# Performance work log

Hardware: AMD Instinct MI355X
Metric: run time of the kernel (lower is better)

The kernel has to match this reference:

```python
import jax, jax.numpy as jnp
import numpy as np

B, S, D = 1, 2048, 1024
E, K, FF = 8, 2, 4096


def setup_inputs() -> dict:
    key = jax.random.key(0)
    ks = jax.random.split(key, 5)
    scale = 1.0 / np.sqrt(D)
    return {
        "hidden_states": jax.random.normal(ks[0], (B, S, D), dtype=jnp.float32),
        "gate_w": jax.random.normal(ks[1], (E, D), dtype=jnp.float32) * scale,
        "w1": jax.random.normal(ks[2], (E, FF, D), dtype=jnp.float32) * scale,
        "w3": jax.random.normal(ks[3], (E, FF, D), dtype=jnp.float32) * scale,
        "w2": jax.random.normal(ks[4], (E, D, FF), dtype=jnp.float32) * (1.0 / np.sqrt(FF)),
    }


def reference(hidden_states, gate_w, w1, w3, w2):
    b, s, d = hidden_states.shape
    h = hidden_states.reshape(-1, d)                       # [T, D]
    T = h.shape[0]

    router_logits = h @ gate_w.T                           # [T, E]
    rw = jax.nn.softmax(router_logits.astype(jnp.float32), axis=-1)
    top_w, top_idx = jax.lax.top_k(rw, K)                  # [T, K]
    top_w = top_w / jnp.sum(top_w, axis=-1, keepdims=True)
    top_w = top_w.astype(h.dtype)

    # combine weights per (token, expert): zero for non-selected experts
    cw = jnp.zeros((T, E), dtype=h.dtype)
    cw = cw.at[jnp.arange(T)[:, None], top_idx].set(top_w)  # [T, E]

    # dense per-expert gated MLP (E is a small fixed set)
    up = jnp.einsum('td,efd->tef', h, w1)                  # [T, E, FF]
    gt = jnp.einsum('td,efd->tef', h, w3)
    inter = jax.nn.silu(up) * gt
    out_e = jnp.einsum('tef,edf->ted', inter, w2)          # [T, E, D]
    out = jnp.einsum('ted,te->td', out_e, cw)              # [T, D]

    return out.reshape(b, s, d), router_logits
```

## Files before the change

kernel.cpp:

```cpp
#include <hip/hip_runtime.h>
#include <hip/hip_bf16.h>
#include <math.h>

#define T_      2048
#define D_      1024
#define E_      8
#define FF_     4096

typedef __attribute__((ext_vector_type(8))) short  bf16x8;
typedef __attribute__((ext_vector_type(4))) float  f32x4;
typedef __attribute__((ext_vector_type(4))) __bf16 b16x4;

static __device__ inline void async_copy16(const void* g, void* l) {
    __builtin_amdgcn_global_load_lds(
        (const __attribute__((address_space(1))) unsigned int*)g,
        (__attribute__((address_space(3))) unsigned int*)l, 16, 0, 0);
}

__global__ __launch_bounds__(256) void cvt_kernel(
    const float4* __restrict__ src, b16x4* __restrict__ dst, int n4)
{
    int i = blockIdx.x * 256 + threadIdx.x;
    int stride = gridDim.x * 256;
    for (; i < n4; i += stride) {
        float4 v = src[i];
        f32x4 vv; vv[0] = v.x; vv[1] = v.y; vv[2] = v.z; vv[3] = v.w;
        dst[i] = __builtin_convertvector(vv, b16x4);
    }
}

__global__ __launch_bounds__(256) void router_kernel(
    const float* __restrict__ h, const float* __restrict__ gw,
    __bf16* __restrict__ hbf, float* __restrict__ logits,
    int* __restrict__ counts, int* __restrict__ lists, float* __restrict__ wlist)
{
    int t = blockIdx.x * 4 + (threadIdx.x >> 6);
    int lane = threadIdx.x & 63;
    const float4* hrow = (const float4*)(h + (size_t)t * D_);
    const float4* gw4  = (const float4*)gw;
    float part[E_];
#pragma unroll
    for (int e = 0; e < E_; ++e) part[e] = 0.f;
#pragma unroll 4
    for (int i = lane; i < 256; i += 64) {
        float4 v = hrow[i];
        f32x4 vv; vv[0] = v.x; vv[1] = v.y; vv[2] = v.z; vv[3] = v.w;
        b16x4 bv = __builtin_convertvector(vv, b16x4);
        *(b16x4*)(hbf + (size_t)t * D_ + i * 4) = bv;
#pragma unroll
        for (int e = 0; e < E_; ++e) {
            float4 g = gw4[e * 256 + i];
            part[e] += v.x * g.x + v.y * g.y + v.z * g.z + v.w * g.w;
        }
    }
#pragma unroll
    for (int e = 0; e < E_; ++e) {
        float v = part[e];
#pragma unroll
        for (int off = 32; off > 0; off >>= 1) v += __shfl_down(v, off, 64);
        part[e] = v;
    }
    if (lane == 0) {
        float* lo = logits + (size_t)t * E_;
#pragma unroll
        for (int e = 0; e < E_; ++e) lo[e] = part[e];
        int i0 = 0;
#pragma unroll
        for (int e = 1; e < E_; ++e) if (part[e] > part[i0]) i0 = e;
        int i1 = (i0 == 0) ? 1 : 0;
#pragma unroll
        for (int e = 0; e < E_; ++e)
            if (e != i0 && part[e] > part[i1]) i1 = e;
        float w1v = expf(part[i1] - part[i0]);
        float s = 1.0f + w1v;
        int p0 = atomicAdd(&counts[i0], 1);
        lists[i0 * T_ + p0] = t; wlist[i0 * T_ + p0] = 1.0f / s;
        int p1 = atomicAdd(&counts[i1], 1);
        lists[i1 * T_ + p1] = t; wlist[i1 * T_ + p1] = w1v / s;
    }
}

__global__ void prefix_kernel(const int* __restrict__ counts, int* __restrict__ offs) {
    if (threadIdx.x == 0) {
        int s = 0;
#pragma unroll
        for (int e = 0; e < E_; ++e) { offs[e] = s; s += counts[e]; }
    }
}

#define G1_SEGS 36
__global__ __launch_bounds__(512, 4) void gemm1_kernel(
    const __bf16* __restrict__ hbf,
    const __bf16* __restrict__ w1b, const __bf16* __restrict__ w3b,
    const int* __restrict__ counts, const int* __restrict__ offs,
    const int* __restrict__ lists, __bf16* __restrict__ inter)
{
    int bid   = blockIdx.x;
    int sx    = bid & 7;
    int rr    = bid >> 3;
    int tile  = rr & 31;
    int sg    = rr >> 5;
    int slice = sg * 8 + sx;
    int nt    = slice & 15;
    int e     = slice >> 4;
    int ne    = counts[e];
    if (tile * 64 >= ne) return;
    int gb = offs[e];

    __shared__ __bf16 sh[2][G1_SEGS * 512];

    int tid = threadIdx.x, lane = tid & 63, w = tid >> 6;
    int ln = lane & 15, q = lane >> 4;
    int r4 = lane >> 2, c4 = lane & 3;

    const __bf16* gs[5];
    int sseg[5];
#pragma unroll
    for (int i = 0; i < 5; ++i) {
        int s = w + i * 8;
        sseg[i] = s;
        gs[i] = hbf;
        if (s < 4) {
            int row = s * 16 + r4;
            int idx = tile * 64 + row; if (idx >= ne) idx = ne - 1;
            int tok = lists[e * T_ + idx];
            gs[i] = hbf + (size_t)tok * D_ + ((c4 ^ ((row >> 1) & 3)) * 8);
        } else if (s < 20) {
            int row = (s - 4) * 16 + r4;
            gs[i] = w1b + ((size_t)e * FF_ + nt * 256 + row) * D_
                        + ((c4 ^ ((row >> 1) & 3)) * 8);
        } else if (s < G1_SEGS) {
            int row = (s - 20) * 16 + r4;
            gs[i] = w3b + ((size_t)e * FF_ + nt * 256 + row) * D_
                        + ((c4 ^ ((row >> 1) & 3)) * 8);
        }
    }

    int cxs = (q ^ ((ln >> 1) & 3)) * 8;
    int aoff[4], boff[2];
#pragma unroll
    for (int mt = 0; mt < 4; ++mt) aoff[mt] = (mt * 16 + ln) * 32 + cxs;
#pragma unroll
    for (int nf = 0; nf < 2; ++nf)
        boff[nf] = 2048 + (w * 32 + nf * 16 + ln) * 32 + cxs;

    f32x4 up[4][2], gt[4][2];
#pragma unroll
    for (int mt = 0; mt < 4; ++mt)
#pragma unroll
        for (int nf = 0; nf < 2; ++nf) {
            up[mt][nf] = (f32x4){0.f, 0.f, 0.f, 0.f};
            gt[mt][nf] = (f32x4){0.f, 0.f, 0.f, 0.f};
        }

#pragma unroll
    for (int i = 0; i < 5; ++i)
        if (sseg[i] < G1_SEGS)
            async_copy16(gs[i], &sh[0][sseg[i] * 512]);
    __syncthreads();

    for (int t = 0; t < 32; ++t) {
        if (t + 1 < 32) {
#pragma unroll
            for (int i = 0; i < 5; ++i)
                if (sseg[i] < G1_SEGS)
                    async_copy16(gs[i] + (t + 1) * 32,
                                 &sh[(t + 1) & 1][sseg[i] * 512]);
        }
        const __bf16* S = sh[t & 1];
        bf16x8 b1[2], b3[2];
#pragma unroll
        for (int nf = 0; nf < 2; ++nf) {
            b1[nf] = *(const bf16x8*)(S + boff[nf]);
            b3[nf] = *(const bf16x8*)(S + boff[nf] + 8192);
        }
#pragma unroll
        for (int mt = 0; mt < 4; ++mt) {
            bf16x8 a = *(const bf16x8*)(S + aoff[mt]);
#pragma unroll
            for (int nf = 0; nf < 2; ++nf) {
                up[mt][nf] = __builtin_amdgcn_mfma_f32_16x16x32_bf16(a, b1[nf], up[mt][nf], 0, 0, 0);
                gt[mt][nf] = __builtin_amdgcn_mfma_f32_16x16x32_bf16(a, b3[nf], gt[mt][nf], 0, 0, 0);
            }
        }
        __syncthreads();
    }

    __bf16* trw = (__bf16*)&sh[0][0] + w * 384;
    int ffb = nt * 256 + w * 32;
#pragma unroll
    for (int mt = 0; mt < 4; ++mt) {
        int idx = tile * 64 + mt * 16 + ln;
#pragma unroll
        for (int nf = 0; nf < 2; ++nf) {
#pragma unroll
            for (int r = 0; r < 4; ++r) {
                float u = up[mt][nf][r], g = gt[mt][nf][r];
                float val = (u / (1.f + expf(-u))) * g;
                trw[(q * 4 + r) * 24 + ln] = (__bf16)val;
            }
            __asm__ volatile("s_waitcnt lgkmcnt(0)" ::: "memory");
            b16x4 v4 = *(b16x4*)&trw[ln * 24 + q * 4];
            if (idx < ne)
                *(b16x4*)(inter + (size_t)(gb + idx) * FF_ + ffb + nf * 16 + q * 4) = v4;
            __asm__ volatile("s_waitcnt lgkmcnt(0)" ::: "memory");
        }
    }
}

#define G2_SEGS 24
__global__ __launch_bounds__(512, 4) void gemm2_kernel(
    const __bf16* __restrict__ inter, const __bf16* __restrict__ w2b,
    const int* __restrict__ counts, const int* __restrict__ offs,
    const int* __restrict__ lists, const float* __restrict__ wlist,
    float* __restrict__ out)
{
    int bid   = blockIdx.x;
    int sx    = bid & 7;
    int rr    = bid >> 3;
    int tile  = rr & 15;
    int sg    = rr >> 4;
    int slice = sg * 8 + sx;
    int ks    = slice & 3;
    int nd    = (slice >> 2) & 3;
    int e     = slice >> 4;
    int ne    = counts[e];
    if (tile * 128 >= ne) return;
    int gb = offs[e];

    __shared__ __bf16 sh[2][G2_SEGS * 512];
    __shared__ int    stok[128];
    __shared__ float  swgt[128];

    int tid = threadIdx.x, lane = tid & 63, w = tid >> 6;
    int ln = lane & 15, q = lane >> 4;
    int r4 = lane >> 2, c4 = lane & 3;
    int wm = w >> 2, wn = w & 3;

    const __bf16* gs[3];
#pragma unroll
    for (int i = 0; i < 3; ++i) {
        int s = w + i * 8;
        if (s < 8) {
            int row = s * 16 + r4;
            int idx = tile * 128 + row; if (idx >= ne) idx = ne - 1;
            gs[i] = inter + (size_t)(gb + idx) * FF_ + ks * 1024
                          + ((c4 ^ ((row >> 1) & 3)) * 8);
        } else {
            int row = (s - 8) * 16 + r4;
            gs[i] = w2b + ((size_t)e * D_ + nd * 256 + row) * FF_ + ks * 1024
                        + ((c4 ^ ((row >> 1) & 3)) * 8);
        }
    }

    int cxs = (q ^ ((ln >> 1) & 3)) * 8;
    int aoff[4], boff[4];
#pragma unroll
    for (int mt = 0; mt < 4; ++mt) aoff[mt] = (wm * 64 + mt * 16 + ln) * 32 + cxs;
#pragma unroll
    for (int nf = 0; nf < 4; ++nf)
        boff[nf] = 4096 + (wn * 64 + nf * 16 + ln) * 32 + cxs;

    f32x4 acc[4][4];
#pragma unroll
    for (int mt = 0; mt < 4; ++mt)
#pragma unroll
        for (int nf = 0; nf < 4; ++nf) acc[mt][nf] = (f32x4){0.f, 0.f, 0.f, 0.f};

#pragma unroll
    for (int i = 0; i < 3; ++i) {
        int s = w + i * 8;
        async_copy16(gs[i], &sh[0][s * 512]);
    }
    if (tid < 128) {
        int idx = tile * 128 + tid;
        int c   = idx < ne ? idx : ne - 1;
        stok[tid] = lists[e * T_ + c];
        swgt[tid] = (idx < ne) ? wlist[e * T_ + idx] : 0.f;
    }
    __syncthreads();

    for (int t = 0; t < 32; ++t) {
        if (t + 1 < 32) {
#pragma unroll
            for (int i = 0; i < 3; ++i) {
                int s = w + i * 8;
                async_copy16(gs[i] + (t + 1) * 32, &sh[(t + 1) & 1][s * 512]);
            }
        }
        const __bf16* S = sh[t & 1];
        bf16x8 b[4];
#pragma unroll
        for (int nf = 0; nf < 4; ++nf) b[nf] = *(const bf16x8*)(S + boff[nf]);
#pragma unroll
        for (int mt = 0; mt < 4; ++mt) {
            bf16x8 a = *(const bf16x8*)(S + aoff[mt]);
#pragma unroll
            for (int nf = 0; nf < 4; ++nf)
                acc[mt][nf] = __builtin_amdgcn_mfma_f32_16x16x32_bf16(a, b[nf], acc[mt][nf], 0, 0, 0);
        }
        __syncthreads();
    }

    int dbase = nd * 256 + wn * 64;
#pragma unroll
    for (int mt = 0; mt < 4; ++mt) {
#pragma unroll
        for (int r = 0; r < 4; ++r) {
            int m = wm * 64 + mt * 16 + q * 4 + r;
            float wgt = swgt[m];
            if (wgt != 0.f) {
                int tok = stok[m];
#pragma unroll
                for (int nf = 0; nf < 4; ++nf)
                    atomicAdd(out + (size_t)tok * D_ + dbase + nf * 16 + ln,
                              wgt * acc[mt][nf][r]);
            }
        }
    }
}

extern "C" void kernel_launch(void* const* d_in, const int* in_sizes, int n_in,
                              void* d_out, int out_size, void* d_ws, size_t ws_size,
                              hipStream_t stream)
{
    const float* h  = (const float*)d_in[0];
    const float* gw = (const float*)d_in[1];
    const float* w1 = (const float*)d_in[2];
    const float* w3 = (const float*)d_in[3];
    const float* w2 = (const float*)d_in[4];

    float* out    = (float*)d_out;
    float* logits = out + (size_t)T_ * D_;

    const size_t W_ELEMS = (size_t)E_ * FF_ * D_;
    char*   ws     = (char*)d_ws;
    size_t  off    = 0;
    int*    counts = (int*)(ws + off); off += 128;
    int*    offs   = (int*)(ws + off); off += 128;
    int*    lists  = (int*)(ws + off); off += (size_t)E_ * T_ * 4;
    float*  wlist  = (float*)(ws + off); off += (size_t)E_ * T_ * 4;
    __bf16* hbf    = (__bf16*)(ws + off); off += (size_t)T_ * D_ * 2;
    __bf16* inter  = (__bf16*)(ws + off); off += (size_t)T_ * 2 * FF_ * 2;
    __bf16* w1b    = (__bf16*)(ws + off); off += W_ELEMS * 2;
    __bf16* w3b    = (__bf16*)(ws + off); off += W_ELEMS * 2;
    __bf16* w2b    = (__bf16*)(ws + off); off += W_ELEMS * 2;
    (void)ws_size;

    hipMemsetAsync(counts, 0, 256, stream);
    hipMemsetAsync(out, 0, (size_t)T_ * D_ * sizeof(float), stream);

    router_kernel<<<T_ / 4, 256, 0, stream>>>(h, gw, hbf, logits, counts, lists, wlist);
    prefix_kernel<<<1, 64, 0, stream>>>(counts, offs);

    int n4 = (int)(W_ELEMS / 4);
    cvt_kernel<<<4096, 256, 0, stream>>>((const float4*)w1, (b16x4*)w1b, n4);
    cvt_kernel<<<4096, 256, 0, stream>>>((const float4*)w3, (b16x4*)w3b, n4);
    cvt_kernel<<<4096, 256, 0, stream>>>((const float4*)w2, (b16x4*)w2b, n4);

    gemm1_kernel<<<32 * 128, 512, 0, stream>>>(hbf, w1b, w3b, counts, offs, lists, inter);
    gemm2_kernel<<<16 * 128, 512, 0, stream>>>(inter, w2b, counts, offs, lists, wlist, out);
}
```

Before: 664.3 us.

## Fuse fp32-to-bf16 weight conversion into GEMM tile loads

Drops the three standalone weight conversion kernels. The GEMM kernels now read fp32 weights directly into registers, convert them to bf16 and write them into swizzled shared memory after the MFMA block, with the next tile's loads issued before compute. The aim is to remove a full extra read and write pass over 3×128MB of fp32 weights. In exchange, weight tiles that several token tiles reuse are fetched in fp32 (twice the bytes) and converted repeatedly, and the loads are now synchronous register loads. It also raises wave priority around the MFMAs.

```diff
diff --git a/kernel.cpp b/kernel.cpp
--- a/kernel.cpp
+++ b/kernel.cpp
@@ -9,6 +9,8 @@
 
 typedef __attribute__((ext_vector_type(8))) short  bf16x8;
 typedef __attribute__((ext_vector_type(4))) float  f32x4;
+typedef __attribute__((ext_vector_type(8))) float  f32x8;
+typedef __attribute__((ext_vector_type(8))) __bf16 b16x8;
 typedef __attribute__((ext_vector_type(4))) __bf16 b16x4;
 
 static __device__ inline void async_copy16(const void* g, void* l) {
@@ -17,16 +19,12 @@
         (__attribute__((address_space(3))) unsigned int*)l, 16, 0, 0);
 }
 
-__global__ __launch_bounds__(256) void cvt_kernel(
-    const float4* __restrict__ src, b16x4* __restrict__ dst, int n4)
-{
-    int i = blockIdx.x * 256 + threadIdx.x;
-    int stride = gridDim.x * 256;
-    for (; i < n4; i += stride) {
-        float4 v = src[i];
-        f32x4 vv; vv[0] = v.x; vv[1] = v.y; vv[2] = v.z; vv[3] = v.w;
-        dst[i] = __builtin_convertvector(vv, b16x4);
-    }
+static __device__ inline bf16x8 cvt8(float4 a, float4 b) {
+    f32x8 x;
+    x[0] = a.x; x[1] = a.y; x[2] = a.z; x[3] = a.w;
+    x[4] = b.x; x[5] = b.y; x[6] = b.z; x[7] = b.w;
+    b16x8 c = __builtin_convertvector(x, b16x8);
+    return *(bf16x8*)&c;
 }
 
 __global__ __launch_bounds__(256) void router_kernel(
@@ -88,10 +86,9 @@
     }
 }
 
-#define G1_SEGS 36
 __global__ __launch_bounds__(512, 4) void gemm1_kernel(
     const __bf16* __restrict__ hbf,
-    const __bf16* __restrict__ w1b, const __bf16* __restrict__ w3b,
+    const float* __restrict__ w1f, const float* __restrict__ w3f,
     const int* __restrict__ counts, const int* __restrict__ offs,
     const int* __restrict__ lists, __bf16* __restrict__ inter)
 {
@@ -107,34 +104,26 @@
     if (tile * 64 >= ne) return;
     int gb = offs[e];
 
-    __shared__ __bf16 sh[2][G1_SEGS * 512];
+    __shared__ __bf16 sh[2][18432];
 
     int tid = threadIdx.x, lane = tid & 63, w = tid >> 6;
     int ln = lane & 15, q = lane >> 4;
     int r4 = lane >> 2, c4 = lane & 3;
 
-    const __bf16* gs[5];
-    int sseg[5];
-#pragma unroll
-    for (int i = 0; i < 5; ++i) {
-        int s = w + i * 8;
-        sseg[i] = s;
-        gs[i] = hbf;
-        if (s < 4) {
-            int row = s * 16 + r4;
-            int idx = tile * 64 + row; if (idx >= ne) idx = ne - 1;
-            int tok = lists[e * T_ + idx];
-            gs[i] = hbf + (size_t)tok * D_ + ((c4 ^ ((row >> 1) & 3)) * 8);
-        } else if (s < 20) {
-            int row = (s - 4) * 16 + r4;
-            gs[i] = w1b + ((size_t)e * FF_ + nt * 256 + row) * D_
-                        + ((c4 ^ ((row >> 1) & 3)) * 8);
-        } else if (s < G1_SEGS) {
-            int row = (s - 20) * 16 + r4;
-            gs[i] = w3b + ((size_t)e * FF_ + nt * 256 + row) * D_
-                        + ((c4 ^ ((row >> 1) & 3)) * 8);
-        }
-    }
+    const __bf16* ga = hbf;
+    if (w < 4) {
+        int row = w * 16 + r4;
+        int idx = tile * 64 + row; if (idx >= ne) idx = ne - 1;
+        int tok = lists[e * T_ + idx];
+        ga = hbf + (size_t)tok * D_ + ((c4 ^ ((row >> 1) & 3)) * 8);
+    }
+
+    int rowb = (w & 3) * 64 + (lane >> 2);
+    const float* wsrc = (w < 4) ? w1f : w3f;
+    const float* gB = wsrc + ((size_t)e * FF_ + nt * 256 + rowb) * D_
+                           + (lane & 3) * 8;
+    int bbase = (w < 4) ? 2048 : 10240;
+    int wswz  = ((lane & 3) ^ ((lane >> 3) & 3)) * 8;
 
     int cxs = (q ^ ((ln >> 1) & 3)) * 8;
     int aoff[4], boff[2];
@@ -153,35 +142,58 @@
             gt[mt][nf] = (f32x4){0.f, 0.f, 0.f, 0.f};
         }
 
-#pragma unroll
-    for (int i = 0; i < 5; ++i)
-        if (sseg[i] < G1_SEGS)
-            async_copy16(gs[i], &sh[0][sseg[i] * 512]);
+    {
+        float4 rb[4][2];
+#pragma unroll
+        for (int u = 0; u < 4; ++u) {
+            const float* p = gB + (size_t)(u * 16) * D_;
+            rb[u][0] = ((const float4*)p)[0];
+            rb[u][1] = ((const float4*)p)[1];
+        }
+        if (w < 4) async_copy16(ga, &sh[0][w * 512]);
+#pragma unroll
+        for (int u = 0; u < 4; ++u)
+            *(bf16x8*)&sh[0][bbase + (rowb + u * 16) * 32 + wswz] =
+                cvt8(rb[u][0], rb[u][1]);
+    }
     __syncthreads();
 
     for (int t = 0; t < 32; ++t) {
+        int p = t & 1;
+        float4 nb[4][2];
         if (t + 1 < 32) {
 #pragma unroll
-            for (int i = 0; i < 5; ++i)
-                if (sseg[i] < G1_SEGS)
-                    async_copy16(gs[i] + (t + 1) * 32,
-                                 &sh[(t + 1) & 1][sseg[i] * 512]);
-        }
-        const __bf16* S = sh[t & 1];
-        bf16x8 b1[2], b3[2];
+            for (int u = 0; u < 4; ++u) {
+                const float* pp = gB + (size_t)(u * 16) * D_ + (t + 1) * 32;
+                nb[u][0] = ((const float4*)pp)[0];
+                nb[u][1] = ((const float4*)pp)[1];
+            }
+            if (w < 4) async_copy16(ga + (t + 1) * 32, &sh[1 - p][w * 512]);
+        }
+        const __bf16* S = sh[p];
+        bf16x8 b1v[2], b3v[2];
 #pragma unroll
         for (int nf = 0; nf < 2; ++nf) {
-            b1[nf] = *(const bf16x8*)(S + boff[nf]);
-            b3[nf] = *(const bf16x8*)(S + boff[nf] + 8192);
-        }
+            b1v[nf] = *(const bf16x8*)(S + boff[nf]);
+            b3v[nf] = *(const bf16x8*)(S + boff[nf] + 8192);
+        }
+        __builtin_amdgcn_s_setprio(1);
 #pragma unroll
         for (int mt = 0; mt < 4; ++mt) {
             bf16x8 a = *(const bf16x8*)(S + aoff[mt]);
 #pragma unroll
             for (int nf = 0; nf < 2; ++nf) {
-                up[mt][nf] = __builtin_amdgcn_mfma_f32_16x16x32_bf16(a, b1[nf], up[mt][nf], 0, 0, 0);
-                gt[mt][nf] = __builtin_amdgcn_mfma_f32_16x16x32_bf16(a, b3[nf], gt[mt][nf], 0, 0, 0);
-            }
+                up[mt][nf] = __builtin_amdgcn_mfma_f32_16x16x32_bf16(a, b1v[nf], up[mt][nf], 0, 0, 0);
+                gt[mt][nf] = __builtin_amdgcn_mfma_f32_16x16x32_bf16(a, b3v[nf], gt[mt][nf], 0, 0, 0);
+            }
+        }
+        __builtin_amdgcn_s_setprio(0);
+        __builtin_amdgcn_sched_barrier(0);
+        if (t + 1 < 32) {
+#pragma unroll
+            for (int u = 0; u < 4; ++u)
+                *(bf16x8*)&sh[1 - p][bbase + (rowb + u * 16) * 32 + wswz] =
+                    cvt8(nb[u][0], nb[u][1]);
         }
         __syncthreads();
     }
@@ -208,9 +220,8 @@
     }
 }
 
-#define G2_SEGS 24
 __global__ __launch_bounds__(512, 4) void gemm2_kernel(
-    const __bf16* __restrict__ inter, const __bf16* __restrict__ w2b,
+    const __bf16* __restrict__ inter, const float* __restrict__ w2f,
     const int* __restrict__ counts, const int* __restrict__ offs,
     const int* __restrict__ lists, const float* __restrict__ wlist,
     float* __restrict__ out)
@@ -228,7 +239,7 @@
     if (tile * 128 >= ne) return;
     int gb = offs[e];
 
-    __shared__ __bf16 sh[2][G2_SEGS * 512];
+    __shared__ __bf16 sh[2][12288];
     __shared__ int    stok[128];
     __shared__ float  swgt[128];
 
@@ -237,21 +248,18 @@
     int r4 = lane >> 2, c4 = lane & 3;
     int wm = w >> 2, wn = w & 3;
 
-    const __bf16* gs[3];
-#pragma unroll
-    for (int i = 0; i < 3; ++i) {
-        int s = w + i * 8;
-        if (s < 8) {
-            int row = s * 16 + r4;
-            int idx = tile * 128 + row; if (idx >= ne) idx = ne - 1;
-            gs[i] = inter + (size_t)(gb + idx) * FF_ + ks * 1024
-                          + ((c4 ^ ((row >> 1) & 3)) * 8);
-        } else {
-            int row = (s - 8) * 16 + r4;
-            gs[i] = w2b + ((size_t)e * D_ + nd * 256 + row) * FF_ + ks * 1024
-                        + ((c4 ^ ((row >> 1) & 3)) * 8);
-        }
-    }
+    const __bf16* ga;
+    {
+        int row = w * 16 + r4;
+        int idx = tile * 128 + row; if (idx >= ne) idx = ne - 1;
+        ga = inter + (size_t)(gb + idx) * FF_ + ks * 1024
+                   + ((c4 ^ ((row >> 1) & 3)) * 8);
+    }
+
+    int rowb = w * 32 + (lane >> 2);
+    const float* gB = w2f + ((size_t)e * D_ + nd * 256 + rowb) * FF_
+                          + ks * 1024 + (lane & 3) * 8;
+    int wswz = ((lane & 3) ^ ((lane >> 3) & 3)) * 8;
 
     int cxs = (q ^ ((ln >> 1) & 3)) * 8;
     int aoff[4], boff[4];
@@ -267,10 +275,19 @@
 #pragma unroll
         for (int nf = 0; nf < 4; ++nf) acc[mt][nf] = (f32x4){0.f, 0.f, 0.f, 0.f};
 
-#pragma unroll
-    for (int i = 0; i < 3; ++i) {
-        int s = w + i * 8;
-        async_copy16(gs[i], &sh[0][s * 512]);
+    {
+        float4 rb[2][2];
+#pragma unroll
+        for (int u = 0; u < 2; ++u) {
+            const float* p = gB + (size_t)(u * 16) * FF_;
+            rb[u][0] = ((const float4*)p)[0];
+            rb[u][1] = ((const float4*)p)[1];
+        }
+        async_copy16(ga, &sh[0][w * 512]);
+#pragma unroll
+        for (int u = 0; u < 2; ++u)
+            *(bf16x8*)&sh[0][4096 + (rowb + u * 16) * 32 + wswz] =
+                cvt8(rb[u][0], rb[u][1]);
     }
     if (tid < 128) {
         int idx = tile * 128 + tid;
@@ -281,23 +298,36 @@
     __syncthreads();
 
     for (int t = 0; t < 32; ++t) {
+        int p = t & 1;
+        float4 nb[2][2];
         if (t + 1 < 32) {
 #pragma unroll
-            for (int i = 0; i < 3; ++i) {
-                int s = w + i * 8;
-                async_copy16(gs[i] + (t + 1) * 32, &sh[(t + 1) & 1][s * 512]);
-            }
-        }
-        const __bf16* S = sh[t & 1];
+            for (int u = 0; u < 2; ++u) {
+                const float* pp = gB + (size_t)(u * 16) * FF_ + (t + 1) * 32;
+                nb[u][0] = ((const float4*)pp)[0];
+                nb[u][1] = ((const float4*)pp)[1];
+            }
+            async_copy16(ga + (t + 1) * 32, &sh[1 - p][w * 512]);
+        }
+        const __bf16* S = sh[p];
         bf16x8 b[4];
 #pragma unroll
         for (int nf = 0; nf < 4; ++nf) b[nf] = *(const bf16x8*)(S + boff[nf]);
+        __builtin_amdgcn_s_setprio(1);
 #pragma unroll
         for (int mt = 0; mt < 4; ++mt) {
             bf16x8 a = *(const bf16x8*)(S + aoff[mt]);
 #pragma unroll
             for (int nf = 0; nf < 4; ++nf)
                 acc[mt][nf] = __builtin_amdgcn_mfma_f32_16x16x32_bf16(a, b[nf], acc[mt][nf], 0, 0, 0);
+        }
+        __builtin_amdgcn_s_setprio(0);
+        __builtin_amdgcn_sched_barrier(0);
+        if (t + 1 < 32) {
+#pragma unroll
+            for (int u = 0; u < 2; ++u)
+                *(bf16x8*)&sh[1 - p][4096 + (rowb + u * 16) * 32 + wswz] =
+                    cvt8(nb[u][0], nb[u][1]);
         }
         __syncthreads();
     }
@@ -333,7 +363,6 @@
     float* out    = (float*)d_out;
     float* logits = out + (size_t)T_ * D_;
 
-    const size_t W_ELEMS = (size_t)E_ * FF_ * D_;
     char*   ws     = (char*)d_ws;
     size_t  off    = 0;
     int*    counts = (int*)(ws + off); off += 128;
@@ -342,9 +371,6 @@
     float*  wlist  = (float*)(ws + off); off += (size_t)E_ * T_ * 4;
     __bf16* hbf    = (__bf16*)(ws + off); off += (size_t)T_ * D_ * 2;
     __bf16* inter  = (__bf16*)(ws + off); off += (size_t)T_ * 2 * FF_ * 2;
-    __bf16* w1b    = (__bf16*)(ws + off); off += W_ELEMS * 2;
-    __bf16* w3b    = (__bf16*)(ws + off); off += W_ELEMS * 2;
-    __bf16* w2b    = (__bf16*)(ws + off); off += W_ELEMS * 2;
     (void)ws_size;
 
     hipMemsetAsync(counts, 0, 256, stream);
@@ -353,11 +379,6 @@
     router_kernel<<<T_ / 4, 256, 0, stream>>>(h, gw, hbf, logits, counts, lists, wlist);
     prefix_kernel<<<1, 64, 0, stream>>>(counts, offs);
 
-    int n4 = (int)(W_ELEMS / 4);
-    cvt_kernel<<<4096, 256, 0, stream>>>((const float4*)w1, (b16x4*)w1b, n4);
-    cvt_kernel<<<4096, 256, 0, stream>>>((const float4*)w3, (b16x4*)w3b, n4);
-    cvt_kernel<<<4096, 256, 0, stream>>>((const float4*)w2, (b16x4*)w2b, n4);
-
-    gemm1_kernel<<<32 * 128, 512, 0, stream>>>(hbf, w1b, w3b, counts, offs, lists, inter);
-    gemm2_kernel<<<16 * 128, 512, 0, stream>>>(inter, w2b, counts, offs, lists, wlist, out);
-}
+    gemm1_kernel<<<32 * 128, 512, 0, stream>>>(hbf, w1, w3, counts, offs, lists, inter);
+    gemm2_kernel<<<16 * 128, 512, 0, stream>>>(inter, w2, counts, offs, lists, wlist, out);
+}
```

Result: no change. 668.3 us (+0.6%).
